# Kernel optimization log

Measured on AMD Instinct MI355X. Metric: run time of the kernel, lower is better.

The kernel has to match this reference:

```python
import jax, jax.numpy as jnp
import numpy as np

HUGE = jnp.float32(1e31)   # ops.HUGE_INT
EPS = 1e-20
B, AN = 1024, 256
D = 256            # emb_dim
HD = 512           # history_dim
AD = 2 * D         # action_dim
NE, NR = 100000, 400


def setup_inputs() -> dict:
    key = jax.random.key(0)
    ks = jax.random.split(key, 12)
    e = jax.random.randint(ks[0], (B,), 0, NE)
    q = jax.random.randint(ks[1], (B,), 0, NR)
    hstate = jax.random.normal(ks[2], (B, HD), dtype=jnp.float32)
    r_space = jax.random.randint(ks[3], (B, AN), 0, NR)
    e_space = jax.random.randint(ks[4], (B, AN), 0, NE)
    # binary action mask; guarantee at least one valid action per row
    action_mask = (jax.random.uniform(ks[5], (B, AN)) > 0.2).astype(jnp.float32)
    action_mask = action_mask.at[:, 0].set(1.0)
    entity_emb = jax.random.normal(ks[6], (NE, D), dtype=jnp.float32) * 0.02
    relation_emb = jax.random.normal(ks[7], (NR, D), dtype=jnp.float32) * 0.02
    W1 = jax.random.normal(ks[8], (2 * D + HD, AD), dtype=jnp.float32) * (1.0 / np.sqrt(2 * D + HD))
    b1 = jnp.zeros((AD,), dtype=jnp.float32)
    W2 = jax.random.normal(ks[9], (AD, AD), dtype=jnp.float32) * (1.0 / np.sqrt(AD))
    b2 = jnp.zeros((AD,), dtype=jnp.float32)
    return {"e": e, "q": q, "hstate": hstate, "r_space": r_space,
            "e_space": e_space, "action_mask": action_mask,
            "entity_emb": entity_emb, "relation_emb": relation_emb,
            "W1": W1, "b1": b1, "W2": W2, "b2": b2}


def reference(e, q, hstate, r_space, e_space, action_mask,
              entity_emb, relation_emb, W1, b1, W2, b2):
    Q = relation_emb[q]                       # [B, D]
    E = entity_emb[e]                         # [B, D]
    X = jnp.concatenate([E, hstate, Q], axis=-1)          # [B, 2D+HD]
    X = jax.nn.relu(X @ W1 + b1)                          # [B, AD]
    X2 = X @ W2 + b2                                      # [B, AD]
    # action embeddings: [rel_emb[r]; ent_emb[e]] per padded action slot
    A = jnp.concatenate([relation_emb[r_space], entity_emb[e_space]], axis=-1)  # [B, AN, AD]
    scores = jnp.einsum('bad,bd->ba', A, X2) - (1.0 - action_mask) * HUGE      # [B, AN]
    action_dist = jax.nn.softmax(scores, axis=-1)
    entropy = -jnp.sum(action_dist * jnp.log(jnp.clip(action_dist, EPS)), axis=-1)  # [B]
    return action_dist, entropy
```

## Files before the change

kernel.cpp:

```cpp
#include <hip/hip_runtime.h>
#include <math.h>

#define NB   1024
#define NACT 256
#define DIM  256
#define HDIM 512
#define ADIM 512
#define KTOT 1024
#define NE   100000
#define NR   400
#define NRP  448
#define NCAT 704

typedef __attribute__((ext_vector_type(8))) short bf16x8;
typedef __attribute__((ext_vector_type(4))) float f32x4;

__device__ __forceinline__ unsigned short f2bf(float f) {
    unsigned int u = __float_as_uint(f);
    u += 0x7FFF + ((u >> 16) & 1);
    return (unsigned short)(u >> 16);
}
__device__ __forceinline__ ushort4 cvt4(float4 v) {
    ushort4 o = {f2bf(v.x), f2bf(v.y), f2bf(v.z), f2bf(v.w)};
    return o;
}

__global__ __launch_bounds__(256) void prep_kernel(
    const float* __restrict__ W1, const float* __restrict__ W2,
    const float* __restrict__ rel, const float* __restrict__ b2,
    ushort* __restrict__ W1T, ushort* __restrict__ Bcat,
    ushort* __restrict__ W2lowbf, ushort* __restrict__ relbf,
    float* __restrict__ cvec)
{
    const int blk = blockIdx.x, tid = threadIdx.x;
    if (blk < 160) {
        __shared__ float t[64][68];
        const float* in; ushort* out; int Kd, k0, n0, rowbase;
        if (blk < 128) {
            in = W1; out = W1T; Kd = 1024;
            k0 = (blk >> 3) * 64; n0 = (blk & 7) * 64; rowbase = n0;
        } else {
            const int l = blk - 128;
            in = W2; out = Bcat; Kd = 512;
            k0 = (l >> 2) * 64; n0 = 256 + (l & 3) * 64; rowbase = n0 - 256;
        }
        const int kr = tid >> 2, c = tid & 3;
        #pragma unroll
        for (int j = 0; j < 4; ++j) {
            const float4 v = *(const float4*)(in + (size_t)(k0 + kr) * ADIM + n0 + c * 16 + j * 4);
            *(float4*)&t[kr][c * 16 + j * 4] = v;
        }
        __syncthreads();
        const int nr = tid >> 2;
        ushort tmp[16];
        #pragma unroll
        for (int kk = 0; kk < 16; ++kk) tmp[kk] = f2bf(t[c * 16 + kk][nr]);
        *(uint4*)(out + (size_t)(rowbase + nr) * Kd + k0 + c * 16)     = *(uint4*)&tmp[0];
        *(uint4*)(out + (size_t)(rowbase + nr) * Kd + k0 + c * 16 + 8) = *(uint4*)&tmp[8];
    } else if (blk < 288) {
        const int l = blk - 160;
        const int row = l * 4 + (tid >> 6);
        const int d4  = tid & 63;
        const float4 v = *(const float4*)(W2 + (size_t)row * ADIM + d4 * 4);
        *(ushort4*)(W2lowbf + (size_t)row * DIM + d4 * 4) = cvt4(v);
    } else if (blk < 388) {
        const int j = (blk - 288) * 256 + tid;
        ((ushort4*)relbf)[j] = cvt4(((const float4*)rel)[j]);
    } else {
        const int r = (blk - 388) * 256 + tid;
        if (r < NRP) {
            const int rr = (r < NR) ? r : (NR - 1);
            const float* a = rel + (size_t)rr * DIM;
            float s = 0.f;
            for (int d = 0; d < DIM; d += 4) {
                const float4 av = *(const float4*)(a + d);
                const float4 bv = *(const float4*)(b2 + d);
                s += av.x * bv.x + av.y * bv.y + av.z * bv.z + av.w * bv.w;
            }
            cvec[r] = s;
        }
    }
}

__global__ __launch_bounds__(256) void mega2_kernel(
    const float* __restrict__ ent, const float* __restrict__ rel,
    const float* __restrict__ hstate,
    const int* __restrict__ e, const int* __restrict__ q,
    const ushort* __restrict__ W1T, const ushort* __restrict__ relbf,
    const ushort* __restrict__ W2lowbf,
    ushort* __restrict__ Bcat, float* __restrict__ Hpart)
{
    __shared__ __align__(16) ushort Als[64][40];
    __shared__ __align__(16) ushort Bls[64][40];
    const int blk = blockIdx.x, tid = threadIdx.x;
    const int wave = tid >> 6, lane = tid & 63;
    const int qq   = lane >> 4, l15 = lane & 15;
    const int sm   = tid >> 2, sc = tid & 3;

    f32x4 acc[4];
    #pragma unroll
    for (int mt = 0; mt < 4; ++mt) acc[mt] = (f32x4){0.f, 0.f, 0.f, 0.f};

    if (blk < 56) {
        const int n0 = (blk & 7) * 64;
        const int m0 = (blk >> 3) * 64;
        const int arow = (m0 + sm < NR) ? (m0 + sm) : (NR - 1);
        const uint4* ga = (const uint4*)(relbf + (size_t)arow * DIM) + sc;
        const uint4* gb = (const uint4*)(W2lowbf + (size_t)(n0 + sm) * DIM) + sc;
        uint4 pa = ga[0], pb = gb[0];
        for (int it = 0; it < DIM / 32; ++it) {
            *(uint4*)&Als[sm][sc * 8] = pa;
            *(uint4*)&Bls[sm][sc * 8] = pb;
            __syncthreads();
            if (it + 1 < DIM / 32) { pa = ga[(it + 1) * 4]; pb = gb[(it + 1) * 4]; }
            const bf16x8 bfrag = *(const bf16x8*)&Bls[wave * 16 + l15][qq * 8];
            #pragma unroll
            for (int mt = 0; mt < 4; ++mt) {
                const bf16x8 afrag = *(const bf16x8*)&Als[mt * 16 + l15][qq * 8];
                acc[mt] = __builtin_amdgcn_mfma_f32_16x16x32_bf16(afrag, bfrag, acc[mt], 0, 0, 0);
            }
            __syncthreads();
        }
        const int n = n0 + wave * 16 + l15;
        #pragma unroll
        for (int mt = 0; mt < 4; ++mt)
            #pragma unroll
            for (int r = 0; r < 4; ++r) {
                const int m = m0 + mt * 16 + qq * 4 + r;
                Bcat[(size_t)(256 + m) * ADIM + n] = f2bf(acc[mt][r]);
            }
        return;
    }

    const int g  = blk - 56;
    const int n0 = (g & 7) * 64;
    const int m0 = ((g >> 3) & 15) * 64;
    const int z  = g >> 7;
    const int kbase = z * 256;
    const int kofs  = sc * 8;

    const int row = m0 + sm;
    const float* abase;
    if (z == 0)      abase = ent + (size_t)e[row] * DIM;
    else if (z == 3) abase = rel + (size_t)q[row] * DIM;
    else             abase = hstate + (size_t)row * HDIM + (kbase - DIM);
    const uint4* gb = (const uint4*)(W1T + (size_t)(n0 + sm) * KTOT + kbase) + sc;

    float4 pa0 = *(const float4*)(abase + kofs);
    float4 pa1 = *(const float4*)(abase + kofs + 4);
    uint4  pb  = gb[0];

    for (int it = 0; it < 8; ++it) {
        ushort t8[8];
        t8[0] = f2bf(pa0.x); t8[1] = f2bf(pa0.y); t8[2] = f2bf(pa0.z); t8[3] = f2bf(pa0.w);
        t8[4] = f2bf(pa1.x); t8[5] = f2bf(pa1.y); t8[6] = f2bf(pa1.z); t8[7] = f2bf(pa1.w);
        *(uint4*)&Als[sm][sc * 8] = *(uint4*)t8;
        *(uint4*)&Bls[sm][sc * 8] = pb;
        __syncthreads();
        if (it + 1 < 8) {
            const int lofs = (it + 1) * 32 + kofs;
            pa0 = *(const float4*)(abase + lofs);
            pa1 = *(const float4*)(abase + lofs + 4);
            pb  = gb[(it + 1) * 4];
        }
        const bf16x8 bfrag = *(const bf16x8*)&Bls[wave * 16 + l15][qq * 8];
        #pragma unroll
        for (int mt = 0; mt < 4; ++mt) {
            const bf16x8 afrag = *(const bf16x8*)&Als[mt * 16 + l15][qq * 8];
            acc[mt] = __builtin_amdgcn_mfma_f32_16x16x32_bf16(afrag, bfrag, acc[mt], 0, 0, 0);
        }
        __syncthreads();
    }
    float* dst = Hpart + (size_t)z * NB * ADIM;
    const int n = n0 + wave * 16 + l15;
    #pragma unroll
    for (int mt = 0; mt < 4; ++mt)
        #pragma unroll
        for (int r = 0; r < 4; ++r) {
            const int m = m0 + mt * 16 + qq * 4 + r;
            dst[(size_t)m * ADIM + n] = acc[mt][r];
        }
}

__global__ __launch_bounds__(256) void gemm2big(
    const float* __restrict__ Hpart, const float* __restrict__ b1,
    const ushort* __restrict__ Bcat, const float* __restrict__ b2,
    const float* __restrict__ cvec,
    float* __restrict__ X2upPart, float* __restrict__ RtabPart)
{
    __shared__ __align__(16) ushort Als[64][40];
    __shared__ __align__(16) ushort Bls[64][40];
    const int tid  = threadIdx.x;
    const int n0   = blockIdx.x * 64;
    const int m0   = blockIdx.y * 64;
    const int z    = blockIdx.z;
    const int kb   = z * 256;
    const int wave = tid >> 6, lane = tid & 63;
    const int qq   = lane >> 4, l15 = lane & 15;
    const int sm   = tid >> 2, sc = tid & 3;

    const size_t arow = (size_t)(m0 + sm) * ADIM + kb;
    const uint4* gbp = (const uint4*)(Bcat + (size_t)(n0 + sm) * ADIM + kb) + sc;

    f32x4 acc[4];
    #pragma unroll
    for (int mt = 0; mt < 4; ++mt) acc[mt] = (f32x4){0.f, 0.f, 0.f, 0.f};

    float4 pz[4][2], pb1[2];
    uint4  pbv;
    {
        const int lk = sc * 8;
        pb1[0] = *(const float4*)(b1 + kb + lk);
        pb1[1] = *(const float4*)(b1 + kb + lk + 4);
        #pragma unroll
        for (int z4 = 0; z4 < 4; ++z4) {
            const float* hp = Hpart + (size_t)z4 * NB * ADIM + arow + lk;
            pz[z4][0] = *(const float4*)hp;
            pz[z4][1] = *(const float4*)(hp + 4);
        }
        pbv = gbp[0];
    }

    for (int it = 0; it < 8; ++it) {
        float4 s0 = pb1[0], s1 = pb1[1];
        #pragma unroll
        for (int z4 = 0; z4 < 4; ++z4) {
            s0.x += pz[z4][0].x; s0.y += pz[z4][0].y; s0.z += pz[z4][0].z; s0.w += pz[z4][0].w;
            s1.x += pz[z4][1].x; s1.y += pz[z4][1].y; s1.z += pz[z4][1].z; s1.w += pz[z4][1].w;
        }
        ushort t8[8];
        t8[0] = f2bf(fmaxf(s0.x, 0.f)); t8[1] = f2bf(fmaxf(s0.y, 0.f));
        t8[2] = f2bf(fmaxf(s0.z, 0.f)); t8[3] = f2bf(fmaxf(s0.w, 0.f));
        t8[4] = f2bf(fmaxf(s1.x, 0.f)); t8[5] = f2bf(fmaxf(s1.y, 0.f));
        t8[6] = f2bf(fmaxf(s1.z, 0.f)); t8[7] = f2bf(fmaxf(s1.w, 0.f));
        *(uint4*)&Als[sm][sc * 8] = *(uint4*)t8;
        *(uint4*)&Bls[sm][sc * 8] = pbv;
        __syncthreads();
        if (it + 1 < 8) {
            const int lk = (it + 1) * 32 + sc * 8;
            pb1[0] = *(const float4*)(b1 + kb + lk);
            pb1[1] = *(const float4*)(b1 + kb + lk + 4);
            #pragma unroll
            for (int z4 = 0; z4 < 4; ++z4) {
                const float* hp = Hpart + (size_t)z4 * NB * ADIM + arow + lk;
                pz[z4][0] = *(const float4*)hp;
                pz[z4][1] = *(const float4*)(hp + 4);
            }
            pbv = gbp[(it + 1) * 4];
        }
        const bf16x8 bfrag = *(const bf16x8*)&Bls[wave * 16 + l15][qq * 8];
        #pragma unroll
        for (int mt = 0; mt < 4; ++mt) {
            const bf16x8 afrag = *(const bf16x8*)&Als[mt * 16 + l15][qq * 8];
            acc[mt] = __builtin_amdgcn_mfma_f32_16x16x32_bf16(afrag, bfrag, acc[mt], 0, 0, 0);
        }
        __syncthreads();
    }
    const int n = n0 + wave * 16 + l15;
    const float extra = (z == 0) ? ((n < 256) ? b2[256 + n] : cvec[n - 256]) : 0.0f;
    #pragma unroll
    for (int mt = 0; mt < 4; ++mt)
        #pragma unroll
        for (int r = 0; r < 4; ++r) {
            const int m = m0 + mt * 16 + qq * 4 + r;
            const float v = acc[mt][r] + extra;
            if (n < 256) X2upPart[(size_t)z * NB * DIM + (size_t)m * DIM + n] = v;
            else         RtabPart[(size_t)z * NB * NRP + (size_t)m * NRP + (n - 256)] = v;
        }
}

__global__ __launch_bounds__(512) void scores_kernel(
    const int* __restrict__ r_space, const int* __restrict__ e_space,
    const float* __restrict__ amask,
    const float* __restrict__ ent,
    const float* __restrict__ RtabPart, const float* __restrict__ X2upPart,
    float* __restrict__ dist_out, float* __restrict__ ent_out)
{
    const int b    = blockIdx.x;
    const int tid  = threadIdx.x;
    const int wave = tid >> 6;
    const int lane = tid & 63;

    __shared__ float xs[DIM];
    __shared__ float sc[NACT];
    __shared__ int   ridx[NACT];
    __shared__ int   eidx[NACT];
    __shared__ float red1[8], red2[8], red3[8];

    if (tid < NACT) ridx[tid] = r_space[(size_t)b * NACT + tid];
    else            eidx[tid - NACT] = e_space[(size_t)b * NACT + tid - NACT];
    if (tid < DIM / 4) {
        float4 v0 = ((const float4*)(X2upPart + (size_t)b * DIM))[tid];
        const float4 v1 = ((const float4*)(X2upPart + (size_t)NB * DIM + (size_t)b * DIM))[tid];
        v0.x += v1.x; v0.y += v1.y; v0.z += v1.z; v0.w += v1.w;
        ((float4*)xs)[tid] = v0;
    }
    __syncthreads();

    const float4 xe = ((const float4*)xs)[lane];
    const float* R0 = RtabPart + (size_t)b * NRP;
    const float* R1 = RtabPart + (size_t)NB * NRP + (size_t)b * NRP;

    const int abase = wave * 32;
    for (int a0 = abase; a0 < abase + 32; a0 += 16) {
        float rsc = 0.0f;
        if (lane < 16) {
            const int ri = ridx[a0 + lane];
            rsc = R0[ri] + R1[ri];
        }
        float4 ev[16];
        #pragma unroll
        for (int i = 0; i < 16; ++i)
            ev[i] = ((const float4*)(ent + (size_t)eidx[a0 + i] * DIM))[lane];
        float p[16];
        #pragma unroll
        for (int i = 0; i < 16; ++i)
            p[i] = ev[i].x * xe.x + ev[i].y * xe.y + ev[i].z * xe.z + ev[i].w * xe.w;
        #pragma unroll
        for (int off = 32; off; off >>= 1) {
            #pragma unroll
            for (int i = 0; i < 16; ++i) p[i] += __shfl_xor(p[i], off);
        }
        float out = p[0];
        #pragma unroll
        for (int i = 1; i < 16; ++i) out = (lane == i) ? p[i] : out;
        if (lane < 16) sc[a0 + lane] = out + rsc;
    }
    __syncthreads();

    float s = -3.0e38f;
    if (tid < NACT) {
        const float m = amask[(size_t)b * NACT + tid];
        s = sc[tid] - (1.0f - m) * 1e31f;
    }

    float mx = s;
    #pragma unroll
    for (int off = 32; off; off >>= 1) mx = fmaxf(mx, __shfl_xor(mx, off));
    if (lane == 0) red1[wave] = mx;
    __syncthreads();
    mx = red1[0];
    #pragma unroll
    for (int w = 1; w < 8; ++w) mx = fmaxf(mx, red1[w]);

    const float ex = (tid < NACT) ? expf(s - mx) : 0.0f;
    float sum = ex;
    #pragma unroll
    for (int off = 32; off; off >>= 1) sum += __shfl_xor(sum, off);
    if (lane == 0) red2[wave] = sum;
    __syncthreads();
    sum = ((red2[0] + red2[1]) + (red2[2] + red2[3]))
        + ((red2[4] + red2[5]) + (red2[6] + red2[7]));

    const float d = ex / sum;
    if (tid < NACT) dist_out[(size_t)b * NACT + tid] = d;

    float t = (tid < NACT) ? d * logf(fmaxf(d, 1e-20f)) : 0.0f;
    #pragma unroll
    for (int off = 32; off; off >>= 1) t += __shfl_xor(t, off);
    if (lane == 0) red3[wave] = t;
    __syncthreads();
    if (tid == 0)
        ent_out[b] = -(((red3[0] + red3[1]) + (red3[2] + red3[3]))
                     + ((red3[4] + red3[5]) + (red3[6] + red3[7])));
}

extern "C" void kernel_launch(void* const* d_in, const int* in_sizes, int n_in,
                              void* d_out, int out_size, void* d_ws, size_t ws_size,
                              hipStream_t stream) {
    const int*   e       = (const int*)d_in[0];
    const int*   q       = (const int*)d_in[1];
    const float* hstate  = (const float*)d_in[2];
    const int*   r_space = (const int*)d_in[3];
    const int*   e_space = (const int*)d_in[4];
    const float* amask   = (const float*)d_in[5];
    const float* ent     = (const float*)d_in[6];
    const float* rel     = (const float*)d_in[7];
    const float* W1      = (const float*)d_in[8];
    const float* b1      = (const float*)d_in[9];
    const float* W2      = (const float*)d_in[10];
    const float* b2      = (const float*)d_in[11];

    ushort* W1T    = (ushort*)d_ws;
    ushort* Bcat   = W1T    + (size_t)ADIM * KTOT;
    ushort* W2low  = Bcat   + (size_t)NCAT * ADIM;
    ushort* relbf  = W2low  + (size_t)ADIM * DIM;
    float*  cvec   = (float*)(relbf + (size_t)NR * DIM);
    float*  Hpart  = cvec   + NRP;
    float*  X2upP  = Hpart  + (size_t)4 * NB * ADIM;
    float*  RtabP  = X2upP  + (size_t)2 * NB * DIM;
    float*  dist   = (float*)d_out;
    float*  entr   = dist + (size_t)NB * NACT;

    prep_kernel<<<390, 256, 0, stream>>>(W1, W2, rel, b2, W1T, Bcat, W2low, relbf, cvec);
    mega2_kernel<<<568, 256, 0, stream>>>(ent, rel, hstate, e, q, W1T, relbf, W2low, Bcat, Hpart);
    gemm2big<<<dim3(11, 16, 2), 256, 0, stream>>>(Hpart, b1, Bcat, b2, cvec, X2upP, RtabP);
    scores_kernel<<<NB, 512, 0, stream>>>(
        r_space, e_space, amask, ent, RtabP, X2upP, dist, entr);
}
```

Baseline: 223.0 us.

## Pre-reduce split-K partials to bf16 and restructure scores to one thread per action

Adds a reduce_x kernel that sums the four split-K partials of the first GEMM, applies bias and ReLU, and stores a bf16 activation matrix once. Previously every gemm2big block reloaded and re-reduced the fp32 partials redundantly across its 11 N-tiles. gemm2big now streams bf16 A tiles directly. The scores kernel moves to 256 threads, each computing a full 256-wide dot product for one action, with the relation table staged in shared memory; this replaces the cross-lane shuffle reductions but makes each thread read a whole embedding row, so loads are less coalesced. It also adds one extra kernel launch.

Measured after the change: 232.0 us. 4.0% more time.

```diff
diff --git a/kernel.cpp b/kernel.cpp
--- a/kernel.cpp
+++ b/kernel.cpp
@@ -182,10 +182,26 @@
         }
 }
 
+__global__ __launch_bounds__(256) void reduce_x(
+    const float* __restrict__ Hpart, const float* __restrict__ b1,
+    ushort* __restrict__ Xbf)
+{
+    const int i = blockIdx.x * 256 + threadIdx.x;
+    const int col4 = i & (ADIM / 4 - 1);
+    float4 s = ((const float4*)b1)[col4];
+    #pragma unroll
+    for (int z = 0; z < 4; ++z) {
+        const float4 h = ((const float4*)(Hpart + (size_t)z * NB * ADIM))[i];
+        s.x += h.x; s.y += h.y; s.z += h.z; s.w += h.w;
+    }
+    s.x = fmaxf(s.x, 0.f); s.y = fmaxf(s.y, 0.f);
+    s.z = fmaxf(s.z, 0.f); s.w = fmaxf(s.w, 0.f);
+    ((ushort4*)Xbf)[i] = cvt4(s);
+}
+
 __global__ __launch_bounds__(256) void gemm2big(
-    const float* __restrict__ Hpart, const float* __restrict__ b1,
-    const ushort* __restrict__ Bcat, const float* __restrict__ b2,
-    const float* __restrict__ cvec,
+    const ushort* __restrict__ Xbf, const ushort* __restrict__ Bcat,
+    const float* __restrict__ b2, const float* __restrict__ cvec,
     float* __restrict__ X2upPart, float* __restrict__ RtabPart)
 {
     __shared__ __align__(16) ushort Als[64][40];
@@ -199,55 +215,19 @@
     const int qq   = lane >> 4, l15 = lane & 15;
     const int sm   = tid >> 2, sc = tid & 3;
 
-    const size_t arow = (size_t)(m0 + sm) * ADIM + kb;
+    const uint4* gap = (const uint4*)(Xbf  + (size_t)(m0 + sm) * ADIM + kb) + sc;
     const uint4* gbp = (const uint4*)(Bcat + (size_t)(n0 + sm) * ADIM + kb) + sc;
 
     f32x4 acc[4];
     #pragma unroll
     for (int mt = 0; mt < 4; ++mt) acc[mt] = (f32x4){0.f, 0.f, 0.f, 0.f};
 
-    float4 pz[4][2], pb1[2];
-    uint4  pbv;
-    {
-        const int lk = sc * 8;
-        pb1[0] = *(const float4*)(b1 + kb + lk);
-        pb1[1] = *(const float4*)(b1 + kb + lk + 4);
-        #pragma unroll
-        for (int z4 = 0; z4 < 4; ++z4) {
-            const float* hp = Hpart + (size_t)z4 * NB * ADIM + arow + lk;
-            pz[z4][0] = *(const float4*)hp;
-            pz[z4][1] = *(const float4*)(hp + 4);
-        }
-        pbv = gbp[0];
-    }
-
+    uint4 pa = gap[0], pb = gbp[0];
     for (int it = 0; it < 8; ++it) {
-        float4 s0 = pb1[0], s1 = pb1[1];
-        #pragma unroll
-        for (int z4 = 0; z4 < 4; ++z4) {
-            s0.x += pz[z4][0].x; s0.y += pz[z4][0].y; s0.z += pz[z4][0].z; s0.w += pz[z4][0].w;
-            s1.x += pz[z4][1].x; s1.y += pz[z4][1].y; s1.z += pz[z4][1].z; s1.w += pz[z4][1].w;
-        }
-        ushort t8[8];
-        t8[0] = f2bf(fmaxf(s0.x, 0.f)); t8[1] = f2bf(fmaxf(s0.y, 0.f));
-        t8[2] = f2bf(fmaxf(s0.z, 0.f)); t8[3] = f2bf(fmaxf(s0.w, 0.f));
-        t8[4] = f2bf(fmaxf(s1.x, 0.f)); t8[5] = f2bf(fmaxf(s1.y, 0.f));
-        t8[6] = f2bf(fmaxf(s1.z, 0.f)); t8[7] = f2bf(fmaxf(s1.w, 0.f));
-        *(uint4*)&Als[sm][sc * 8] = *(uint4*)t8;
-        *(uint4*)&Bls[sm][sc * 8] = pbv;
-        __syncthreads();
-        if (it + 1 < 8) {
-            const int lk = (it + 1) * 32 + sc * 8;
-            pb1[0] = *(const float4*)(b1 + kb + lk);
-            pb1[1] = *(const float4*)(b1 + kb + lk + 4);
-            #pragma unroll
-            for (int z4 = 0; z4 < 4; ++z4) {
-                const float* hp = Hpart + (size_t)z4 * NB * ADIM + arow + lk;
-                pz[z4][0] = *(const float4*)hp;
-                pz[z4][1] = *(const float4*)(hp + 4);
-            }
-            pbv = gbp[(it + 1) * 4];
-        }
+        *(uint4*)&Als[sm][sc * 8] = pa;
+        *(uint4*)&Bls[sm][sc * 8] = pb;
+        __syncthreads();
+        if (it + 1 < 8) { pa = gap[(it + 1) * 4]; pb = gbp[(it + 1) * 4]; }
         const bf16x8 bfrag = *(const bf16x8*)&Bls[wave * 16 + l15][qq * 8];
         #pragma unroll
         for (int mt = 0; mt < 4; ++mt) {
@@ -269,7 +249,7 @@
         }
 }
 
-__global__ __launch_bounds__(512) void scores_kernel(
+__global__ __launch_bounds__(256) void scores_kernel(
     const int* __restrict__ r_space, const int* __restrict__ e_space,
     const float* __restrict__ amask,
     const float* __restrict__ ent,
@@ -282,87 +262,65 @@
     const int lane = tid & 63;
 
     __shared__ float xs[DIM];
-    __shared__ float sc[NACT];
-    __shared__ int   ridx[NACT];
-    __shared__ int   eidx[NACT];
-    __shared__ float red1[8], red2[8], red3[8];
-
-    if (tid < NACT) ridx[tid] = r_space[(size_t)b * NACT + tid];
-    else            eidx[tid - NACT] = e_space[(size_t)b * NACT + tid - NACT];
-    if (tid < DIM / 4) {
-        float4 v0 = ((const float4*)(X2upPart + (size_t)b * DIM))[tid];
-        const float4 v1 = ((const float4*)(X2upPart + (size_t)NB * DIM + (size_t)b * DIM))[tid];
+    __shared__ float rtab[NRP];
+    __shared__ float red1[4], red2[4], red3[4];
+
+    if (tid < 112) {
+        const float4 v0 = ((const float4*)(RtabPart + (size_t)b * NRP))[tid];
+        const float4 v1 = ((const float4*)(RtabPart + (size_t)NB * NRP + (size_t)b * NRP))[tid];
+        float4 s; s.x = v0.x + v1.x; s.y = v0.y + v1.y; s.z = v0.z + v1.z; s.w = v0.w + v1.w;
+        ((float4*)rtab)[tid] = s;
+    } else if (tid >= 128 && tid < 192) {
+        const int j = tid - 128;
+        float4 v0 = ((const float4*)(X2upPart + (size_t)b * DIM))[j];
+        const float4 v1 = ((const float4*)(X2upPart + (size_t)NB * DIM + (size_t)b * DIM))[j];
         v0.x += v1.x; v0.y += v1.y; v0.z += v1.z; v0.w += v1.w;
-        ((float4*)xs)[tid] = v0;
-    }
+        ((float4*)xs)[j] = v0;
+    }
+    const int   ri  = r_space[(size_t)b * NACT + tid];
+    const int   ei  = e_space[(size_t)b * NACT + tid];
+    const float msk = amask[(size_t)b * NACT + tid];
     __syncthreads();
 
-    const float4 xe = ((const float4*)xs)[lane];
-    const float* R0 = RtabPart + (size_t)b * NRP;
-    const float* R1 = RtabPart + (size_t)NB * NRP + (size_t)b * NRP;
-
-    const int abase = wave * 32;
-    for (int a0 = abase; a0 < abase + 32; a0 += 16) {
-        float rsc = 0.0f;
-        if (lane < 16) {
-            const int ri = ridx[a0 + lane];
-            rsc = R0[ri] + R1[ri];
-        }
-        float4 ev[16];
-        #pragma unroll
-        for (int i = 0; i < 16; ++i)
-            ev[i] = ((const float4*)(ent + (size_t)eidx[a0 + i] * DIM))[lane];
-        float p[16];
-        #pragma unroll
-        for (int i = 0; i < 16; ++i)
-            p[i] = ev[i].x * xe.x + ev[i].y * xe.y + ev[i].z * xe.z + ev[i].w * xe.w;
-        #pragma unroll
-        for (int off = 32; off; off >>= 1) {
-            #pragma unroll
-            for (int i = 0; i < 16; ++i) p[i] += __shfl_xor(p[i], off);
-        }
-        float out = p[0];
-        #pragma unroll
-        for (int i = 1; i < 16; ++i) out = (lane == i) ? p[i] : out;
-        if (lane < 16) sc[a0 + lane] = out + rsc;
-    }
-    __syncthreads();
-
-    float s = -3.0e38f;
-    if (tid < NACT) {
-        const float m = amask[(size_t)b * NACT + tid];
-        s = sc[tid] - (1.0f - m) * 1e31f;
-    }
+    const float4* erow = (const float4*)(ent + (size_t)ei * DIM);
+    const float4* xv4  = (const float4*)xs;
+    float p0 = 0.f, p1 = 0.f, p2 = 0.f, p3 = 0.f;
+    #pragma unroll 2
+    for (int d = 0; d < DIM / 4; d += 4) {
+        const float4 e0 = erow[d], e1 = erow[d + 1], e2 = erow[d + 2], e3 = erow[d + 3];
+        const float4 x0 = xv4[d],  x1 = xv4[d + 1],  x2 = xv4[d + 2],  x3 = xv4[d + 3];
+        p0 += e0.x * x0.x + e0.y * x0.y + e0.z * x0.z + e0.w * x0.w;
+        p1 += e1.x * x1.x + e1.y * x1.y + e1.z * x1.z + e1.w * x1.w;
+        p2 += e2.x * x2.x + e2.y * x2.y + e2.z * x2.z + e2.w * x2.w;
+        p3 += e3.x * x3.x + e3.y * x3.y + e3.z * x3.z + e3.w * x3.w;
+    }
+    const float s = rtab[ri] + ((p0 + p1) + (p2 + p3)) - (1.0f - msk) * 1e31f;
 
     float mx = s;
     #pragma unroll
     for (int off = 32; off; off >>= 1) mx = fmaxf(mx, __shfl_xor(mx, off));
     if (lane == 0) red1[wave] = mx;
     __syncthreads();
-    mx = red1[0];
-    #pragma unroll
-    for (int w = 1; w < 8; ++w) mx = fmaxf(mx, red1[w]);
-
-    const float ex = (tid < NACT) ? expf(s - mx) : 0.0f;
+    mx = fmaxf(fmaxf(red1[0], red1[1]), fmaxf(red1[2], red1[3]));
+
+    const float ex = expf(s - mx);
     float sum = ex;
     #pragma unroll
     for (int off = 32; off; off >>= 1) sum += __shfl_xor(sum, off);
     if (lane == 0) red2[wave] = sum;
     __syncthreads();
-    sum = ((red2[0] + red2[1]) + (red2[2] + red2[3]))
-        + ((red2[4] + red2[5]) + (red2[6] + red2[7]));
+    sum = (red2[0] + red2[1]) + (red2[2] + red2[3]);
 
     const float d = ex / sum;
-    if (tid < NACT) dist_out[(size_t)b * NACT + tid] = d;
-
-    float t = (tid < NACT) ? d * logf(fmaxf(d, 1e-20f)) : 0.0f;
+    dist_out[(size_t)b * NACT + tid] = d;
+
+    float t = d * logf(fmaxf(d, 1e-20f));
     #pragma unroll
     for (int off = 32; off; off >>= 1) t += __shfl_xor(t, off);
     if (lane == 0) red3[wave] = t;
     __syncthreads();
     if (tid == 0)
-        ent_out[b] = -(((red3[0] + red3[1]) + (red3[2] + red3[3]))
-                     + ((red3[4] + red3[5]) + (red3[6] + red3[7])));
+        ent_out[b] = -((red3[0] + red3[1]) + (red3[2] + red3[3]));
 }
 
 extern "C" void kernel_launch(void* const* d_in, const int* in_sizes, int n_in,
@@ -387,14 +345,16 @@
     ushort* relbf  = W2low  + (size_t)ADIM * DIM;
     float*  cvec   = (float*)(relbf + (size_t)NR * DIM);
     float*  Hpart  = cvec   + NRP;
-    float*  X2upP  = Hpart  + (size_t)4 * NB * ADIM;
+    ushort* Xbf    = (ushort*)(Hpart + (size_t)4 * NB * ADIM);
+    float*  X2upP  = (float*)(Xbf + (size_t)NB * ADIM);
     float*  RtabP  = X2upP  + (size_t)2 * NB * DIM;
     float*  dist   = (float*)d_out;
     float*  entr   = dist + (size_t)NB * NACT;
 
     prep_kernel<<<390, 256, 0, stream>>>(W1, W2, rel, b2, W1T, Bcat, W2low, relbf, cvec);
     mega2_kernel<<<568, 256, 0, stream>>>(ent, rel, hstate, e, q, W1T, relbf, W2low, Bcat, Hpart);
-    gemm2big<<<dim3(11, 16, 2), 256, 0, stream>>>(Hpart, b1, Bcat, b2, cvec, X2upP, RtabP);
-    scores_kernel<<<NB, 512, 0, stream>>>(
+    reduce_x<<<512, 256, 0, stream>>>(Hpart, b1, Xbf);
+    gemm2big<<<dim3(11, 16, 2), 256, 0, stream>>>(Xbf, Bcat, b2, cvec, X2upP, RtabP);
+    scores_kernel<<<NB, 256, 0, stream>>>(
         r_space, e_space, amask, ent, RtabP, X2upP, dist, entr);
 }
```
